# Optimization experiments

Hardware: AMD Instinct MI355X
Metric: run time of the kernel (lower is better)

## Reference

```python
import jax, jax.numpy as jnp
import numpy as np

DIM = 2048
H = 16
HD = DIM // H          # 128
ROPE_CH = (HD // 2) // 2 * 2  # 64
EPS = 1e-6
SCALE = HD ** -0.5
MAX_WAVELENGTH = 10000.0


def rmsnorm(v, w):
    vf = v.astype(jnp.float32)
    var = jnp.mean(vf * vf, axis=-1, keepdims=True)
    return (w * (vf * jax.lax.rsqrt(var + EPS))).astype(v.dtype)


def apply_rope(v, pos):
    # v: [B, S, H, C], pos: [B, S]
    C = v.shape[-1]
    frac = 2.0 * jnp.arange(C // 2, dtype=jnp.float32) / C
    timescale = MAX_WAVELENGTH ** frac                      # [C/2]
    ang = pos[:, :, None].astype(jnp.float32) / timescale   # [B, S, C/2]
    ang = ang[:, :, None, :]                                 # [B, S, 1, C/2]
    sin, cos = jnp.sin(ang), jnp.cos(ang)
    v1, v2 = jnp.split(v, 2, axis=-1)
    return jnp.concatenate([v1 * cos - v2 * sin, v2 * cos + v1 * sin], axis=-1).astype(v.dtype)


def apply_rotary_emb(v, pos, channels):
    # rope only the last `channels` of head_dim
    left, right = v[..., :-channels], v[..., -channels:]
    return jnp.concatenate([left, apply_rope(right, pos)], axis=-1)


def project_qkv(t, W, b, qn, kn):
    B, N, _ = t.shape
    qkv = t @ W + b                                          # [B, N, 3*H*HD]
    q, k, v = jnp.split(qkv, [H * HD, 2 * H * HD], axis=-1)
    q = rmsnorm(q.reshape(B, N, H, HD), qn)
    k = rmsnorm(k.reshape(B, N, H, HD), kn)
    v = v.reshape(B, N, H, HD)
    return q, k, v


def setup_inputs() -> dict:
    key = jax.random.key(0)
    ks = jax.random.split(key, 12)
    B, NX, NY = 2, 2048, 512
    x = jax.random.normal(ks[0], (B, NX, DIM), dtype=jnp.float32)
    y = jax.random.normal(ks[1], (B, NY, DIM), dtype=jnp.float32)
    temporal_pos = jax.random.randint(ks[2], (B, NX), 0, 2048)
    y_temporal_pos = jax.random.randint(ks[3], (B, NY), 0, 512)
    s = 0.02
    Wqkv_x = jax.random.normal(ks[4], (DIM, 3 * H * HD), dtype=jnp.float32) * s
    bqkv_x = jnp.zeros((3 * H * HD,), dtype=jnp.float32)
    Wqkv_y = jax.random.normal(ks[5], (DIM, 3 * H * HD), dtype=jnp.float32) * s
    bqkv_y = jnp.zeros((3 * H * HD,), dtype=jnp.float32)
    Wproj_x = jax.random.normal(ks[6], (DIM, DIM), dtype=jnp.float32) * s
    bproj_x = jnp.zeros((DIM,), dtype=jnp.float32)
    Wproj_y = jax.random.normal(ks[7], (DIM, DIM), dtype=jnp.float32) * s
    bproj_y = jnp.zeros((DIM,), dtype=jnp.float32)
    qnx = jnp.ones((HD,), dtype=jnp.float32)
    knx = jnp.ones((HD,), dtype=jnp.float32)
    qny = jnp.ones((HD,), dtype=jnp.float32)
    kny = jnp.ones((HD,), dtype=jnp.float32)
    return {"x": x, "y": y, "temporal_pos": temporal_pos, "y_temporal_pos": y_temporal_pos,
            "Wqkv_x": Wqkv_x, "bqkv_x": bqkv_x, "qnx": qnx, "knx": knx,
            "Wproj_x": Wproj_x, "bproj_x": bproj_x,
            "Wqkv_y": Wqkv_y, "bqkv_y": bqkv_y, "qny": qny, "kny": kny,
            "Wproj_y": Wproj_y, "bproj_y": bproj_y}


def reference(x, y, temporal_pos, y_temporal_pos,
              Wqkv_x, bqkv_x, qnx, knx, Wproj_x, bproj_x,
              Wqkv_y, bqkv_y, qny, kny, Wproj_y, bproj_y):
    B, NX, _ = x.shape
    NY = y.shape[1]
    qx, kx, vx = project_qkv(x, Wqkv_x, bqkv_x, qnx, knx)   # [B, NX, H, HD]
    qy, ky, vy = project_qkv(y, Wqkv_y, bqkv_y, qny, kny)   # [B, NY, H, HD]
    # RoPE on last ROPE_CH channels of head_dim (rope_dim=-1)
    qx = apply_rotary_emb(qx, temporal_pos, ROPE_CH)
    kx = apply_rotary_emb(kx, temporal_pos, ROPE_CH)
    qy = apply_rotary_emb(qy, y_temporal_pos, ROPE_CH)
    ky = apply_rotary_emb(ky, y_temporal_pos, ROPE_CH)
    # joint attention over concatenated x/y tokens
    q = jnp.concatenate([qx, qy], axis=1)   # [B, S, H, HD]
    k = jnp.concatenate([kx, ky], axis=1)
    v = jnp.concatenate([vx, vy], axis=1)
    scores = jnp.einsum('bqhd,bkhd->bhqk', q, k) * SCALE
    attn = jax.nn.softmax(scores, axis=-1)
    out = jnp.einsum('bhqk,bkhd->bqhd', attn, v)             # [B, S, H, HD]
    out = out.reshape(B, NX + NY, DIM).astype(x.dtype)
    x_out = out[:, :NX] @ Wproj_x + bproj_x
    y_out = out[:, NX:] @ Wproj_y + bproj_y
    return (x_out, y_out)
```

## Files before the change

### kernel.cpp

```cpp
#include <hip/hip_runtime.h>
#include <stdint.h>

typedef __attribute__((ext_vector_type(8))) short v8s;
typedef __attribute__((ext_vector_type(4))) float v4f;

#define DEV static __device__ __forceinline__

DEV unsigned short f2bf(float f) {
  union { float f; unsigned int u; } v; v.f = f;
  unsigned int u = v.u;
  return (unsigned short)((u + 0x7fffu + ((u >> 16) & 1u)) >> 16);
}

DEV v4f mfma16(v8s a, v8s b, v4f c) {
  return __builtin_amdgcn_mfma_f32_16x16x32_bf16(a, b, c, 0, 0, 0);
}

DEV unsigned int cvtpk(float lo, float hi) {
  unsigned int r;
  asm("v_cvt_pk_bf16_f32 %0, %1, %2" : "=v"(r) : "v"(lo), "v"(hi));
  return r;
}

DEV void async16(const void* g, void* lds) {
  __builtin_amdgcn_global_load_lds((const __attribute__((address_space(1))) unsigned int*)g,
                                   (__attribute__((address_space(3))) unsigned int*)lds,
                                   16, 0, 0);
}

__global__ __launch_bounds__(256) void k_f32_to_bf16(const float* __restrict__ in,
                                                     unsigned short* __restrict__ out, int n4) {
  int i = blockIdx.x * 256 + threadIdx.x;
  if (i < n4) {
    float4 v = reinterpret_cast<const float4*>(in)[i];
    ushort4 o;
    o.x = f2bf(v.x); o.y = f2bf(v.y); o.z = f2bf(v.z); o.w = f2bf(v.w);
    reinterpret_cast<ushort4*>(out)[i] = o;
  }
}

__global__ __launch_bounds__(256) void k_rope_tbl(const int* __restrict__ pos,
                                                  float* __restrict__ tbl, int nrows) {
  int idx = blockIdx.x * 256 + threadIdx.x;
  if (idx < nrows * 32) {
    int row = idx >> 5, i = idx & 31;
    float ang = (float)pos[row] * expf((float)i * -0.2878231366f);
    float sv, cv;
    sincosf(ang, &sv, &cv);
    reinterpret_cast<float2*>(tbl)[(size_t)row * 32 + i] = make_float2(cv, sv);
  }
}

__global__ __launch_bounds__(256) void k_transpose(const float* __restrict__ in,
                                                   unsigned short* __restrict__ out, int R, int C) {
  __shared__ float tile[64][65];
  const int r0 = blockIdx.x * 64, c0 = blockIdx.y * 64;
  const int t = threadIdx.x;
  const int rl = t >> 4, cl = (t & 15) * 4;
#pragma unroll
  for (int p = 0; p < 4; p++) {
    const int r = rl + p * 16;
    float4 v = *reinterpret_cast<const float4*>(&in[(size_t)(r0 + r) * C + c0 + cl]);
    tile[r][cl] = v.x; tile[r][cl + 1] = v.y; tile[r][cl + 2] = v.z; tile[r][cl + 3] = v.w;
  }
  __syncthreads();
  const int cw = t >> 4, rw = (t & 15) * 4;
#pragma unroll
  for (int p = 0; p < 4; p++) {
    const int c = cw + p * 16;
    ushort4 o;
    o.x = f2bf(tile[rw + 0][c]); o.y = f2bf(tile[rw + 1][c]);
    o.z = f2bf(tile[rw + 2][c]); o.w = f2bf(tile[rw + 3][c]);
    *reinterpret_cast<ushort4*>(&out[(size_t)(c0 + c) * R + r0 + rw]) = o;
  }
}

template <int MODE>
__global__ __launch_bounds__(512, 4) void k_gemm(
    const unsigned short* __restrict__ A, const unsigned short* __restrict__ Bt,
    const float* __restrict__ bias, float* __restrict__ Cout,
    unsigned short* __restrict__ Qb, unsigned short* __restrict__ Kb,
    unsigned short* __restrict__ Vt, const float* __restrict__ qn,
    const float* __restrict__ kn, const float* __restrict__ rtbl, int K, int N, int Nm, int noff,
    int rows_per_b, int b_stride, int row_off, int Mb) {
  __shared__ __align__(16) char Lds[3 * 24576];
  const int chunk = gridDim.x >> 3;
  const int o = (blockIdx.x & 7) * chunk + (blockIdx.x >> 3);
  const int m0 = (o % Mb) * 128, n0 = (o / Mb) * 256;
  const int t = threadIdx.x, l = t & 63, w = t >> 6;
  const int lg = l >> 4, li = l & 15;
  const int wr = w >> 1, wc = w & 1;

  auto amap = [&](int m) -> size_t {
    return (size_t)(m / rows_per_b) * b_stride + row_off + (m % rows_per_b);
  };
  const int ar = t >> 2, as = t & 3;
  const int asw = (as ^ ((ar >> 1) & 3)) * 8;
  const unsigned short* ap = A + amap(m0 + ar) * K + asw;
  const unsigned short* bp0 = Bt + (size_t)(n0 + ar) * K + asw;
  const unsigned short* bp1 = bp0 + (size_t)128 * K;
  const int t16 = t * 16;

  auto stage = [&](char* lb, int st) {
    const int ko = st * 32;
    async16(ap + ko, lb + t16);
    async16(bp0 + ko, lb + 8192 + t16);
    async16(bp1 + ko, lb + 16384 + t16);
  };

  int aoff[2], boff[8];
#pragma unroll
  for (int mf = 0; mf < 2; mf++) {
    const int row = wr * 32 + mf * 16 + li;
    aoff[mf] = row * 64 + ((lg ^ ((row >> 1) & 3)) * 16);
  }
#pragma unroll
  for (int nf = 0; nf < 8; nf++) {
    const int row = wc * 128 + nf * 16 + li;
    boff[nf] = 8192 + row * 64 + ((lg ^ ((row >> 1) & 3)) * 16);
  }

  v4f acc[2][8] = {};
  const int NK = K >> 5;

  stage(Lds, 0);
  stage(Lds + 24576, 1);
  stage(Lds + 49152, 2);

  int bufc = 0;
  for (int tt = 0; tt < NK; tt++) {
    asm volatile("s_waitcnt vmcnt(6)" ::: "memory");
    __builtin_amdgcn_sched_barrier(0);
    __builtin_amdgcn_s_barrier();
    __builtin_amdgcn_sched_barrier(0);
    char* Bf = Lds + bufc;
    v8s af0 = *reinterpret_cast<const v8s*>(Bf + aoff[0]);
    v8s af1 = *reinterpret_cast<const v8s*>(Bf + aoff[1]);
    __builtin_amdgcn_s_setprio(1);
#pragma unroll
    for (int nf = 0; nf < 8; nf++) {
      v8s bfv = *reinterpret_cast<const v8s*>(Bf + boff[nf]);
      acc[0][nf] = mfma16(af0, bfv, acc[0][nf]);
      acc[1][nf] = mfma16(af1, bfv, acc[1][nf]);
    }
    __builtin_amdgcn_s_setprio(0);
    __builtin_amdgcn_sched_barrier(0);
    __builtin_amdgcn_s_barrier();
    __builtin_amdgcn_sched_barrier(0);
    stage(Bf, (tt + 3 < NK) ? tt + 3 : NK - 1);
    bufc += 24576;
    if (bufc == 73728) bufc = 0;
  }
  asm volatile("s_waitcnt vmcnt(0)" ::: "memory");

#pragma unroll
  for (int nf = 0; nf < 8; nf++) {
    const float bv = bias[n0 + wc * 128 + nf * 16 + li];
#pragma unroll
    for (int mf = 0; mf < 2; mf++)
#pragma unroll
      for (int r = 0; r < 4; r++) acc[mf][nf][r] += bv;
  }

  if (MODE == 0) {
#pragma unroll
    for (int mf = 0; mf < 2; mf++) {
      const int row = m0 + wr * 32 + mf * 16 + lg * 4;
#pragma unroll
      for (int nf = 0; nf < 8; nf++) {
        const int col = n0 + wc * 128 + nf * 16 + li;
#pragma unroll
        for (int r = 0; r < 4; r++) Cout[(size_t)(row + r) * N + col] = acc[mf][nf][r];
      }
    }
    return;
  }

  const int sec = n0 >> 11;
  const int hh = ((n0 + wc * 128) >> 7) & 15;
  const int mrow0 = m0 + wr * 32;

  if (sec < 2) {
    const float* gw = (sec == 0) ? qn : kn;
    unsigned short* Out = (sec == 0) ? Qb : Kb;
    float g[8];
#pragma unroll
    for (int nf = 0; nf < 8; nf++) g[nf] = gw[nf * 16 + li];
#pragma unroll
    for (int mf = 0; mf < 2; mf++) {
#pragma unroll
      for (int r = 0; r < 4; r++) {
        float s = 0.f;
#pragma unroll
        for (int nf = 0; nf < 8; nf++) s += acc[mf][nf][r] * acc[mf][nf][r];
#pragma unroll
        for (int off = 1; off < 16; off <<= 1) s += __shfl_xor(s, off, 64);
        const int m = mrow0 + mf * 16 + lg * 4 + r;
        const float rn = rsqrtf(s * (1.0f / 128.0f) + 1e-6f);
        float vv[8];
#pragma unroll
        for (int nf = 0; nf < 8; nf++) vv[nf] = acc[mf][nf][r] * rn * g[nf];
#pragma unroll
        for (int nf = 4; nf < 6; nf++) {
          const float2 cs =
              reinterpret_cast<const float2*>(rtbl)[(size_t)m * 32 + (nf - 4) * 16 + li];
          const float v1 = vv[nf], v2 = vv[nf + 2];
          vv[nf] = v1 * cs.x - v2 * cs.y;
          vv[nf + 2] = v2 * cs.x + v1 * cs.y;
        }
        const int b = m / Nm, n = m - b * Nm;
        const size_t base = ((size_t)(b * 16 + hh) * 2560 + noff + n) * 128;
#pragma unroll
        for (int nf = 0; nf < 8; nf++) Out[base + nf * 16 + li] = f2bf(vv[nf]);
      }
    }
  } else {
#pragma unroll
    for (int mf = 0; mf < 2; mf++) {
      const int m = mrow0 + mf * 16 + lg * 4;
      const int b = m / Nm, n = m - b * Nm;
      const int key = noff + n;
      const size_t base = ((size_t)(b * 16 + hh) * 80 + (key >> 5)) * 4096 + (key & 31);
#pragma unroll
      for (int nf = 0; nf < 8; nf++) {
        const int chan = nf * 16 + li;
        ushort4 ov;
        ov.x = f2bf(acc[mf][nf][0]); ov.y = f2bf(acc[mf][nf][1]);
        ov.z = f2bf(acc[mf][nf][2]); ov.w = f2bf(acc[mf][nf][3]);
        *reinterpret_cast<ushort4*>(&Vt[base + chan * 32]) = ov;
      }
    }
  }
}

__global__ __launch_bounds__(256) void k_attn(const unsigned short* __restrict__ Qb,
                                              const unsigned short* __restrict__ Kb,
                                              const unsigned short* __restrict__ Vt,
                                              unsigned short* __restrict__ Ob) {
  __shared__ __align__(16) char Ldss[3 * 16384];
  const int NT = 2560;
  const float SC = 0.08838834764831845f;
  const float FM = 12.0f;
  const int i = blockIdx.x;
  const int xcd = i & 7, j = i >> 3;
  const int qt = j % 20;
  const int bh = xcd * 4 + j / 20;
  const int b = bh >> 4, h = bh & 15;
  const int t = threadIdx.x, l = t & 63, w = t >> 6;
  const int lg = l >> 4, li = l & 15;
  const unsigned short* Qbase = Qb + ((size_t)bh * NT + qt * 128) * 128;
  const unsigned short* Kbase = Kb + (size_t)bh * NT * 128;
  const unsigned short* Vbase = Vt + (size_t)bh * 327680;

  v8s qf[2][4];
#pragma unroll
  for (int mg = 0; mg < 2; mg++) {
    const int row = w * 32 + mg * 16 + li;
#pragma unroll
    for (int ds = 0; ds < 4; ds++)
      qf[mg][ds] = *reinterpret_cast<const v8s*>(Qbase + (size_t)row * 128 + (lg + ds * 4) * 8);
  }

  auto stage = [&](char* lb, int st) {
#pragma unroll
    for (int p = 0; p < 2; p++) {
      const int rho = w * 4 + (l >> 4) + p * 16;
      const int key = ((rho >> 2) & 3) * 8 + ((rho >> 4) & 1) * 4 + (rho & 3);
      const char* g = (const char*)Kbase + ((size_t)(st * 32 + key)) * 256 +
                      (((l & 15) ^ (rho & 7)) * 16);
      async16(g, lb + w * 1024 + p * 4096);
    }
#pragma unroll
    for (int p = 0; p < 2; p++) {
      const int d = w * 32 + p * 16 + (l >> 2);
      const char* g = (const char*)Vbase + (size_t)st * 8192 + d * 64 +
                      ((((l & 3) * 2) ^ (d & 6)) * 8);
      async16(g, lb + 8192 + w * 2048 + p * 1024);
    }
  };

  int koff[2][4], voff[8];
#pragma unroll
  for (int kf = 0; kf < 2; kf++)
#pragma unroll
    for (int ds = 0; ds < 4; ds++) {
      const int row = kf * 16 + li;
      koff[kf][ds] = row * 256 + (((lg + ds * 4) ^ (row & 7)) * 16);
    }
#pragma unroll
  for (int df = 0; df < 8; df++) {
    const int d = df * 16 + li;
    voff[df] = 8192 + d * 64 + (((lg * 2) ^ (d & 6)) * 8);
  }

  float ps[2] = {0.f, 0.f};
  v4f O_[2][8] = {};

  stage(Ldss, 0);
  stage(Ldss + 16384, 1);
  stage(Ldss + 32768, 2);

  int bufc = 0;
  for (int tt = 0; tt < 80; tt++) {
    asm volatile("s_waitcnt vmcnt(8)" ::: "memory");
    __builtin_amdgcn_sched_barrier(0);
    __builtin_amdgcn_s_barrier();
    __builtin_amdgcn_sched_barrier(0);
    char* B = Ldss + bufc;

    v4f s[2][2] = {};
    __builtin_amdgcn_s_setprio(1);
#pragma unroll
    for (int kf = 0; kf < 2; kf++)
#pragma unroll
      for (int ds = 0; ds < 4; ds++) {
        v8s ka = *reinterpret_cast<const v8s*>(B + koff[kf][ds]);
        s[0][kf] = mfma16(ka, qf[0][ds], s[0][kf]);
        s[1][kf] = mfma16(ka, qf[1][ds], s[1][kf]);
      }
    __builtin_amdgcn_s_setprio(0);

    v8s pa[2];
#pragma unroll
    for (int mg = 0; mg < 2; mg++) {
      float p[2][4];
#pragma unroll
      for (int kf = 0; kf < 2; kf++)
#pragma unroll
        for (int r = 0; r < 4; r++) {
          p[kf][r] = __expf(fmaf(s[mg][kf][r], SC, -FM));
          ps[mg] += p[kf][r];
        }
      union { v8s v; unsigned int u[4]; } pk;
      pk.u[0] = cvtpk(p[0][0], p[0][1]);
      pk.u[1] = cvtpk(p[0][2], p[0][3]);
      pk.u[2] = cvtpk(p[1][0], p[1][1]);
      pk.u[3] = cvtpk(p[1][2], p[1][3]);
      pa[mg] = pk.v;
    }

    __builtin_amdgcn_s_setprio(1);
#pragma unroll
    for (int df = 0; df < 8; df++) {
      v8s vb = *reinterpret_cast<const v8s*>(B + voff[df]);
      O_[0][df] = mfma16(pa[0], vb, O_[0][df]);
      O_[1][df] = mfma16(pa[1], vb, O_[1][df]);
    }
    __builtin_amdgcn_s_setprio(0);

    __builtin_amdgcn_sched_barrier(0);
    __builtin_amdgcn_s_barrier();
    __builtin_amdgcn_sched_barrier(0);
    const int st = (tt + 3 < 80) ? tt + 3 : 79;
    stage(B, st);
    bufc += 16384;
    if (bufc == 49152) bufc = 0;
  }
  asm volatile("s_waitcnt vmcnt(0)" ::: "memory");

#pragma unroll
  for (int mg = 0; mg < 2; mg++) {
    ps[mg] += __shfl_xor(ps[mg], 16, 64);
    ps[mg] += __shfl_xor(ps[mg], 32, 64);
  }
#pragma unroll
  for (int mg = 0; mg < 2; mg++) {
    float inv[4];
#pragma unroll
    for (int r = 0; r < 4; r++) inv[r] = 1.0f / __shfl(ps[mg], lg * 4 + r, 64);
#pragma unroll
    for (int df = 0; df < 8; df++) {
      const int d = df * 16 + li;
#pragma unroll
      for (int r = 0; r < 4; r++) {
        const int q = qt * 128 + w * 32 + mg * 16 + lg * 4 + r;
        Ob[((size_t)b * NT + q) * 2048 + h * 128 + d] = f2bf(O_[mg][df][r] * inv[r]);
      }
    }
  }
}

extern "C" void kernel_launch(void* const* d_in, const int* in_sizes, int n_in,
                              void* d_out, int out_size, void* d_ws, size_t ws_size,
                              hipStream_t stream) {
  (void)in_sizes; (void)n_in; (void)out_size;
  const float* x = (const float*)d_in[0];
  const float* y = (const float*)d_in[1];
  const int* tpos = (const int*)d_in[2];
  const int* ypos = (const int*)d_in[3];
  const float* Wqkv_x = (const float*)d_in[4];
  const float* bqkv_x = (const float*)d_in[5];
  const float* qnx = (const float*)d_in[6];
  const float* knx = (const float*)d_in[7];
  const float* Wproj_x = (const float*)d_in[8];
  const float* bproj_x = (const float*)d_in[9];
  const float* Wqkv_y = (const float*)d_in[10];
  const float* bqkv_y = (const float*)d_in[11];
  const float* qny = (const float*)d_in[12];
  const float* kny = (const float*)d_in[13];
  const float* Wproj_y = (const float*)d_in[14];
  const float* bproj_y = (const float*)d_in[15];
  float* outp = (float*)d_out;

  char* ws = (char*)d_ws;
  size_t off = 0;
  auto alloc = [&](size_t b) {
    char* p = ws + off;
    off += (b + 255) & ~(size_t)255;
    return p;
  };
  unsigned short* Wt = (unsigned short*)alloc(6144ull * 2048 * 2);
  unsigned short* xb = (unsigned short*)alloc(4096ull * 2048 * 2);
  unsigned short* yb = (unsigned short*)alloc(1024ull * 2048 * 2);
  unsigned short* Qbf = (unsigned short*)alloc(2ull * 16 * 2560 * 128 * 2);
  unsigned short* Kbf = (unsigned short*)alloc(2ull * 16 * 2560 * 128 * 2);
  unsigned short* Vtb = (unsigned short*)alloc(2ull * 16 * 80 * 128 * 32 * 2);
  unsigned short* Obf = (unsigned short*)alloc(2ull * 2560 * 2048 * 2);
  float* rtx = (float*)alloc(4096ull * 64 * 4);
  float* rty = (float*)alloc(1024ull * 64 * 4);
  if (ws_size < off) return;

  k_f32_to_bf16<<<8192, 256, 0, stream>>>(x, xb, 2097152);
  k_f32_to_bf16<<<2048, 256, 0, stream>>>(y, yb, 524288);
  k_rope_tbl<<<512, 256, 0, stream>>>(tpos, rtx, 4096);
  k_rope_tbl<<<128, 256, 0, stream>>>(ypos, rty, 1024);

  k_transpose<<<dim3(32, 96), 256, 0, stream>>>(Wqkv_x, Wt, 2048, 6144);
  k_gemm<1><<<768, 512, 0, stream>>>(xb, Wt, bqkv_x, nullptr, Qbf, Kbf, Vtb, qnx, knx, rtx, 2048,
                                     6144, 2048, 0, 4096, 0, 0, 32);
  k_transpose<<<dim3(32, 96), 256, 0, stream>>>(Wqkv_y, Wt, 2048, 6144);
  k_gemm<1><<<192, 512, 0, stream>>>(yb, Wt, bqkv_y, nullptr, Qbf, Kbf, Vtb, qny, kny, rty, 2048,
                                     6144, 512, 2048, 1024, 0, 0, 8);

  k_attn<<<640, 256, 0, stream>>>(Qbf, Kbf, Vtb, Obf);

  k_transpose<<<dim3(32, 32), 256, 0, stream>>>(Wproj_x, Wt, 2048, 2048);
  k_gemm<0><<<256, 512, 0, stream>>>(Obf, Wt, bproj_x, outp, nullptr, nullptr, nullptr, nullptr,
                                     nullptr, nullptr, 2048, 2048, 0, 0, 2048, 2560, 0, 32);
  k_transpose<<<dim3(32, 32), 256, 0, stream>>>(Wproj_y, Wt, 2048, 2048);
  k_gemm<0><<<64, 512, 0, stream>>>(Obf, Wt, bproj_y, outp + 8388608ull, nullptr, nullptr, nullptr,
                                    nullptr, nullptr, nullptr, 2048, 2048, 0, 0, 512, 2560, 2048,
                                    8);
}
```

Measured before the change: 444.2 us.

## Switch attention kernel to 32x32x16 MFMA with reworked LDS layouts

Rewrites the attention inner loop to use 32x32x16 bf16 MFMA instead of 16x16x32. Q fragments, K/V LDS staging layouts, swizzles and the output/normalization epilogue are remapped to match the 32x32 operand layout. The aim is fewer MFMA issues and LDS reads per tile, with more reuse per instruction. The cost is larger accumulators, so register pressure rises, and the new swizzles may cause LDS bank conflicts.

New measurement: 450.6 us. Within noise of the previous version (+1.4%).

```diff
diff --git a/kernel.cpp b/kernel.cpp
--- a/kernel.cpp
+++ b/kernel.cpp
@@ -3,6 +3,7 @@
 
 typedef __attribute__((ext_vector_type(8))) short v8s;
 typedef __attribute__((ext_vector_type(4))) float v4f;
+typedef __attribute__((ext_vector_type(16))) float f32x16;
 
 #define DEV static __device__ __forceinline__
 
@@ -14,6 +15,10 @@
 
 DEV v4f mfma16(v8s a, v8s b, v4f c) {
   return __builtin_amdgcn_mfma_f32_16x16x32_bf16(a, b, c, 0, 0, 0);
+}
+
+DEV f32x16 mfma32(v8s a, v8s b, f32x16 c) {
+  return __builtin_amdgcn_mfma_f32_32x32x16_bf16(a, b, c, 0, 0, 0);
 }
 
 DEV unsigned int cvtpk(float lo, float hi) {
@@ -247,54 +252,46 @@
   const int bh = xcd * 4 + j / 20;
   const int b = bh >> 4, h = bh & 15;
   const int t = threadIdx.x, l = t & 63, w = t >> 6;
-  const int lg = l >> 4, li = l & 15;
+  const int l31 = l & 31, hi = l >> 5;
   const unsigned short* Qbase = Qb + ((size_t)bh * NT + qt * 128) * 128;
   const unsigned short* Kbase = Kb + (size_t)bh * NT * 128;
   const unsigned short* Vbase = Vt + (size_t)bh * 327680;
 
-  v8s qf[2][4];
-#pragma unroll
-  for (int mg = 0; mg < 2; mg++) {
-    const int row = w * 32 + mg * 16 + li;
-#pragma unroll
-    for (int ds = 0; ds < 4; ds++)
-      qf[mg][ds] = *reinterpret_cast<const v8s*>(Qbase + (size_t)row * 128 + (lg + ds * 4) * 8);
+  v8s qf[8];
+  {
+    const unsigned short* qrow = Qbase + (size_t)(w * 32 + l31) * 128 + hi * 8;
+#pragma unroll
+    for (int s = 0; s < 8; s++) qf[s] = *reinterpret_cast<const v8s*>(qrow + s * 16);
   }
 
   auto stage = [&](char* lb, int st) {
 #pragma unroll
     for (int p = 0; p < 2; p++) {
-      const int rho = w * 4 + (l >> 4) + p * 16;
-      const int key = ((rho >> 2) & 3) * 8 + ((rho >> 4) & 1) * 4 + (rho & 3);
+      const int rho = (t >> 4) + p * 16;
+      const int key = (rho & 3) + ((rho >> 3) & 1) * 4 + ((rho >> 2) & 1) * 8 + (rho & 16);
       const char* g = (const char*)Kbase + ((size_t)(st * 32 + key)) * 256 +
-                      (((l & 15) ^ (rho & 7)) * 16);
-      async16(g, lb + w * 1024 + p * 4096);
+                      (((t & 15) ^ (rho & 7)) * 16);
+      async16(g, lb + t * 16 + p * 4096);
     }
 #pragma unroll
     for (int p = 0; p < 2; p++) {
-      const int d = w * 32 + p * 16 + (l >> 2);
+      const int d = (t >> 2) + p * 64;
       const char* g = (const char*)Vbase + (size_t)st * 8192 + d * 64 +
-                      ((((l & 3) * 2) ^ (d & 6)) * 8);
-      async16(g, lb + 8192 + w * 2048 + p * 1024);
+                      (((t & 3) ^ ((d >> 1) & 3)) * 16);
+      async16(g, lb + 8192 + t * 16 + p * 4096);
     }
   };
 
-  int koff[2][4], voff[8];
-#pragma unroll
-  for (int kf = 0; kf < 2; kf++)
-#pragma unroll
-    for (int ds = 0; ds < 4; ds++) {
-      const int row = kf * 16 + li;
-      koff[kf][ds] = row * 256 + (((lg + ds * 4) ^ (row & 7)) * 16);
-    }
-#pragma unroll
-  for (int df = 0; df < 8; df++) {
-    const int d = df * 16 + li;
-    voff[df] = 8192 + d * 64 + (((lg * 2) ^ (d & 6)) * 8);
-  }
-
-  float ps[2] = {0.f, 0.f};
-  v4f O_[2][8] = {};
+  int koff[8], voff[2];
+#pragma unroll
+  for (int s = 0; s < 8; s++)
+    koff[s] = l31 * 256 + (((s * 2 + hi) ^ (l & 7)) * 16);
+#pragma unroll
+  for (int kh = 0; kh < 2; kh++)
+    voff[kh] = 8192 + l31 * 64 + (((kh * 2 + hi) ^ ((l >> 1) & 3)) * 16);
+
+  float ps = 0.f;
+  f32x16 O_[4] = {};
 
   stage(Ldss, 0);
   stage(Ldss + 16384, 1);
@@ -308,74 +305,65 @@
     __builtin_amdgcn_sched_barrier(0);
     char* B = Ldss + bufc;
 
-    v4f s[2][2] = {};
+    f32x16 s_ = {};
     __builtin_amdgcn_s_setprio(1);
 #pragma unroll
-    for (int kf = 0; kf < 2; kf++)
-#pragma unroll
-      for (int ds = 0; ds < 4; ds++) {
-        v8s ka = *reinterpret_cast<const v8s*>(B + koff[kf][ds]);
-        s[0][kf] = mfma16(ka, qf[0][ds], s[0][kf]);
-        s[1][kf] = mfma16(ka, qf[1][ds], s[1][kf]);
+    for (int s = 0; s < 8; s++) {
+      v8s ka = *reinterpret_cast<const v8s*>(B + koff[s]);
+      s_ = mfma32(ka, qf[s], s_);
+    }
+    __builtin_amdgcn_s_setprio(0);
+
+    float p[16];
+#pragma unroll
+    for (int r = 0; r < 16; r++) {
+      p[r] = __expf(fmaf(s_[r], SC, -FM));
+      ps += p[r];
+    }
+    v8s pa[2];
+    union { v8s v; unsigned int u[4]; } pk0, pk1;
+#pragma unroll
+    for (int e = 0; e < 4; e++) {
+      pk0.u[e] = cvtpk(p[e * 2], p[e * 2 + 1]);
+      pk1.u[e] = cvtpk(p[8 + e * 2], p[8 + e * 2 + 1]);
+    }
+    pa[0] = pk0.v;
+    pa[1] = pk1.v;
+
+    __builtin_amdgcn_s_setprio(1);
+#pragma unroll
+    for (int db = 0; db < 4; db++) {
+#pragma unroll
+      for (int kh = 0; kh < 2; kh++) {
+        v8s vb = *reinterpret_cast<const v8s*>(B + db * 2048 + voff[kh]);
+        O_[db] = mfma32(pa[kh], vb, O_[db]);
       }
+    }
     __builtin_amdgcn_s_setprio(0);
 
-    v8s pa[2];
-#pragma unroll
-    for (int mg = 0; mg < 2; mg++) {
-      float p[2][4];
-#pragma unroll
-      for (int kf = 0; kf < 2; kf++)
-#pragma unroll
-        for (int r = 0; r < 4; r++) {
-          p[kf][r] = __expf(fmaf(s[mg][kf][r], SC, -FM));
-          ps[mg] += p[kf][r];
-        }
-      union { v8s v; unsigned int u[4]; } pk;
-      pk.u[0] = cvtpk(p[0][0], p[0][1]);
-      pk.u[1] = cvtpk(p[0][2], p[0][3]);
-      pk.u[2] = cvtpk(p[1][0], p[1][1]);
-      pk.u[3] = cvtpk(p[1][2], p[1][3]);
-      pa[mg] = pk.v;
-    }
-
-    __builtin_amdgcn_s_setprio(1);
-#pragma unroll
-    for (int df = 0; df < 8; df++) {
-      v8s vb = *reinterpret_cast<const v8s*>(B + voff[df]);
-      O_[0][df] = mfma16(pa[0], vb, O_[0][df]);
-      O_[1][df] = mfma16(pa[1], vb, O_[1][df]);
-    }
-    __builtin_amdgcn_s_setprio(0);
-
     __builtin_amdgcn_sched_barrier(0);
     __builtin_amdgcn_s_barrier();
     __builtin_amdgcn_sched_barrier(0);
     const int st = (tt + 3 < 80) ? tt + 3 : 79;
-    stage(B, st);
+    stage(Ldss + bufc, st);
     bufc += 16384;
     if (bufc == 49152) bufc = 0;
   }
   asm volatile("s_waitcnt vmcnt(0)" ::: "memory");
 
-#pragma unroll
-  for (int mg = 0; mg < 2; mg++) {
-    ps[mg] += __shfl_xor(ps[mg], 16, 64);
-    ps[mg] += __shfl_xor(ps[mg], 32, 64);
-  }
-#pragma unroll
-  for (int mg = 0; mg < 2; mg++) {
-    float inv[4];
-#pragma unroll
-    for (int r = 0; r < 4; r++) inv[r] = 1.0f / __shfl(ps[mg], lg * 4 + r, 64);
-#pragma unroll
-    for (int df = 0; df < 8; df++) {
-      const int d = df * 16 + li;
-#pragma unroll
-      for (int r = 0; r < 4; r++) {
-        const int q = qt * 128 + w * 32 + mg * 16 + lg * 4 + r;
-        Ob[((size_t)b * NT + q) * 2048 + h * 128 + d] = f2bf(O_[mg][df][r] * inv[r]);
-      }
+  ps += __shfl_xor(ps, 32, 64);
+  float inv[16];
+#pragma unroll
+  for (int r = 0; r < 16; r++) {
+    const int qrow = (r & 3) + 8 * (r >> 2) + 4 * hi;
+    inv[r] = 1.0f / __shfl(ps, qrow, 64);
+  }
+#pragma unroll
+  for (int db = 0; db < 4; db++) {
+#pragma unroll
+    for (int r = 0; r < 16; r++) {
+      const int q = qt * 128 + w * 32 + (r & 3) + 8 * (r >> 2) + 4 * hi;
+      Ob[((size_t)b * NT + q) * 2048 + h * 128 + db * 32 + l31] = f2bf(O_[db][r] * inv[r]);
     }
   }
 }
```

## Split attention key range across two wave groups and combine partial outputs in LDS

Applied to the files above, without the earlier changes.

The attention kernel now runs 512 threads per block. Each pair of waves shares a 32-row query group and splits every 64-key tile into two 32-key halves, so the loop runs 40 iterations with double buffering instead of 80 with triple buffering. At the end, the second wave of each pair writes its partial O accumulators and row sums to LDS, and the first wave adds them, normalizes and stores. This is meant to double the waves available to hide latency, at the cost of a cross-wave reduction with extra barriers, a shallower prefetch pipeline and tighter register limits from launch_bounds(512,4).

New measurement: 564.4 us. 27.1% more time.

```diff
diff --git a/kernel.cpp b/kernel.cpp
--- a/kernel.cpp
+++ b/kernel.cpp
@@ -233,11 +233,11 @@
   }
 }
 
-__global__ __launch_bounds__(256) void k_attn(const unsigned short* __restrict__ Qb,
-                                              const unsigned short* __restrict__ Kb,
-                                              const unsigned short* __restrict__ Vt,
-                                              unsigned short* __restrict__ Ob) {
-  __shared__ __align__(16) char Ldss[3 * 16384];
+__global__ __launch_bounds__(512, 4) void k_attn(const unsigned short* __restrict__ Qb,
+                                                 const unsigned short* __restrict__ Kb,
+                                                 const unsigned short* __restrict__ Vt,
+                                                 unsigned short* __restrict__ Ob) {
+  __shared__ __align__(16) char Ldss[2 * 32768];
   const int NT = 2560;
   const float SC = 0.08838834764831845f;
   const float FM = 12.0f;
@@ -248,6 +248,7 @@
   const int b = bh >> 4, h = bh & 15;
   const int t = threadIdx.x, l = t & 63, w = t >> 6;
   const int lg = l >> 4, li = l & 15;
+  const int qg = w >> 1, kh = w & 1;
   const unsigned short* Qbase = Qb + ((size_t)bh * NT + qt * 128) * 128;
   const unsigned short* Kbase = Kb + (size_t)bh * NT * 128;
   const unsigned short* Vbase = Vt + (size_t)bh * 327680;
@@ -255,7 +256,7 @@
   v8s qf[2][4];
 #pragma unroll
   for (int mg = 0; mg < 2; mg++) {
-    const int row = w * 32 + mg * 16 + li;
+    const int row = qg * 32 + mg * 16 + li;
 #pragma unroll
     for (int ds = 0; ds < 4; ds++)
       qf[mg][ds] = *reinterpret_cast<const v8s*>(Qbase + (size_t)row * 128 + (lg + ds * 4) * 8);
@@ -264,18 +265,19 @@
   auto stage = [&](char* lb, int st) {
 #pragma unroll
     for (int p = 0; p < 2; p++) {
-      const int rho = w * 4 + (l >> 4) + p * 16;
-      const int key = ((rho >> 2) & 3) * 8 + ((rho >> 4) & 1) * 4 + (rho & 3);
-      const char* g = (const char*)Kbase + ((size_t)(st * 32 + key)) * 256 +
-                      (((l & 15) ^ (rho & 7)) * 16);
-      async16(g, lb + w * 1024 + p * 4096);
+      const int rho = p * 32 + (t >> 4);
+      const int rp = rho & 31;
+      const int key = p * 32 + ((rp >> 2) & 3) * 8 + ((rp >> 4) & 1) * 4 + (rp & 3);
+      const char* g = (const char*)Kbase + ((size_t)(st * 64 + key)) * 256 +
+                      (((t & 15) ^ (rho & 7)) * 16);
+      async16(g, lb + p * 8192 + (t & 511) * 16);
     }
 #pragma unroll
     for (int p = 0; p < 2; p++) {
-      const int d = w * 32 + p * 16 + (l >> 2);
-      const char* g = (const char*)Vbase + (size_t)st * 8192 + d * 64 +
-                      ((((l & 3) * 2) ^ (d & 6)) * 8);
-      async16(g, lb + 8192 + w * 2048 + p * 1024);
+      const int d = t >> 2;
+      const char* g = (const char*)Vbase + ((size_t)(st * 2 + p)) * 8192 + d * 64 +
+                      ((((t & 3) * 2) ^ (d & 6)) * 8);
+      async16(g, lb + 16384 + p * 8192 + (t & 511) * 16);
     }
   };
 
@@ -284,25 +286,24 @@
   for (int kf = 0; kf < 2; kf++)
 #pragma unroll
     for (int ds = 0; ds < 4; ds++) {
-      const int row = kf * 16 + li;
+      const int row = kh * 32 + kf * 16 + li;
       koff[kf][ds] = row * 256 + (((lg + ds * 4) ^ (row & 7)) * 16);
     }
 #pragma unroll
   for (int df = 0; df < 8; df++) {
     const int d = df * 16 + li;
-    voff[df] = 8192 + d * 64 + (((lg * 2) ^ (d & 6)) * 8);
+    voff[df] = 16384 + kh * 8192 + d * 64 + (((lg * 2) ^ (d & 6)) * 8);
   }
 
   float ps[2] = {0.f, 0.f};
   v4f O_[2][8] = {};
 
   stage(Ldss, 0);
-  stage(Ldss + 16384, 1);
-  stage(Ldss + 32768, 2);
+  stage(Ldss + 32768, 1);
 
   int bufc = 0;
-  for (int tt = 0; tt < 80; tt++) {
-    asm volatile("s_waitcnt vmcnt(8)" ::: "memory");
+  for (int tt = 0; tt < 40; tt++) {
+    asm volatile("s_waitcnt vmcnt(4)" ::: "memory");
     __builtin_amdgcn_sched_barrier(0);
     __builtin_amdgcn_s_barrier();
     __builtin_amdgcn_sched_barrier(0);
@@ -351,10 +352,8 @@
     __builtin_amdgcn_sched_barrier(0);
     __builtin_amdgcn_s_barrier();
     __builtin_amdgcn_sched_barrier(0);
-    const int st = (tt + 3 < 80) ? tt + 3 : 79;
-    stage(B, st);
-    bufc += 16384;
-    if (bufc == 49152) bufc = 0;
+    stage(B, (tt + 2 < 40) ? tt + 2 : 39);
+    bufc ^= 32768;
   }
   asm volatile("s_waitcnt vmcnt(0)" ::: "memory");
 
@@ -363,20 +362,37 @@
     ps[mg] += __shfl_xor(ps[mg], 16, 64);
     ps[mg] += __shfl_xor(ps[mg], 32, 64);
   }
+
+  __syncthreads();
+  float* comb = (float*)Ldss;
+  const int cbase = (qg * 64 + l) * 33;
 #pragma unroll
   for (int mg = 0; mg < 2; mg++) {
-    float inv[4];
-#pragma unroll
-    for (int r = 0; r < 4; r++) inv[r] = 1.0f / __shfl(ps[mg], lg * 4 + r, 64);
-#pragma unroll
-    for (int df = 0; df < 8; df++) {
-      const int d = df * 16 + li;
-#pragma unroll
-      for (int r = 0; r < 4; r++) {
-        const int q = qt * 128 + w * 32 + mg * 16 + lg * 4 + r;
-        Ob[((size_t)b * NT + q) * 2048 + h * 128 + d] = f2bf(O_[mg][df][r] * inv[r]);
+    if (kh) {
+#pragma unroll
+      for (int df = 0; df < 8; df++)
+#pragma unroll
+        for (int r = 0; r < 4; r++) comb[cbase + df * 4 + r] = O_[mg][df][r];
+      comb[cbase + 32] = ps[mg];
+    }
+    __syncthreads();
+    if (!kh) {
+      const float pst = ps[mg] + comb[cbase + 32];
+      float inv[4];
+#pragma unroll
+      for (int r = 0; r < 4; r++) inv[r] = 1.0f / __shfl(pst, lg * 4 + r, 64);
+#pragma unroll
+      for (int df = 0; df < 8; df++) {
+        const int d = df * 16 + li;
+#pragma unroll
+        for (int r = 0; r < 4; r++) {
+          const int q = qt * 128 + qg * 32 + mg * 16 + lg * 4 + r;
+          Ob[((size_t)b * NT + q) * 2048 + h * 128 + d] =
+              f2bf((O_[mg][df][r] + comb[cbase + df * 4 + r]) * inv[r]);
+        }
       }
     }
+    __syncthreads();
   }
 }
 
@@ -432,7 +448,7 @@
   k_gemm<1><<<192, 512, 0, stream>>>(yb, Wt, bqkv_y, nullptr, Qbf, Kbf, Vtb, qny, kny, rty, 2048,
                                      6144, 512, 2048, 1024, 0, 0, 8);
 
-  k_attn<<<640, 256, 0, stream>>>(Qbf, Kbf, Vtb, Obf);
+  k_attn<<<640, 512, 0, stream>>>(Qbf, Kbf, Vtb, Obf);
 
   k_transpose<<<dim3(32, 32), 256, 0, stream>>>(Wproj_x, Wt, 2048, 2048);
   k_gemm<0><<<256, 512, 0, stream>>>(Obf, Wt, bproj_x, outp, nullptr, nullptr, nullptr, nullptr,
```
